# Optimization experiments

Hardware: AMD Instinct MI355X
Metric: run time of the kernel (lower is better)

The kernel has to match this reference:

```python
import jax, jax.numpy as jnp
import numpy as np

T, B, V, D, H = 1024, 128, 50257, 128, 512


def _lstm_cell(x, h, c, w_ih, w_hh, b_ih, b_hh):
    # x: [B, D], h/c: [B, H]; gates: [B, 4H] in PyTorch i,f,g,o order
    gates = x @ w_ih.T + h @ w_hh.T + b_ih + b_hh
    i, f, g, o = jnp.split(gates, 4, axis=-1)
    c_new = jax.nn.sigmoid(f) * c + jax.nn.sigmoid(i) * jnp.tanh(g)
    h_new = jax.nn.sigmoid(o) * jnp.tanh(c_new)
    return h_new, c_new


def setup_inputs() -> dict:
    key = jax.random.key(0)
    ks = jax.random.split(key, 7)
    s = 1.0 / np.sqrt(H)
    return {
        "input_ids": jax.random.randint(ks[0], (T, B), 0, V),
        "seq_len": jnp.sort(jax.random.randint(ks[1], (B,), 0, T)),
        "emb_weight": jax.random.normal(ks[2], (V, D), jnp.float32) * 0.1,
        "w_ih": jax.random.uniform(ks[3], (4 * H, D), jnp.float32, -s, s),
        "w_hh": jax.random.uniform(ks[4], (4 * H, H), jnp.float32, -s, s),
        "b_ih": jax.random.uniform(ks[5], (4 * H,), jnp.float32, -s, s),
        "b_hh": jax.random.uniform(ks[6], (4 * H,), jnp.float32, -s, s),
    }


def reference(input_ids, seq_len, emb_weight, w_ih, w_hh, b_ih, b_hh):
    Tn, Bn = input_ids.shape
    Hn = w_hh.shape[1]
    dt = emb_weight.dtype
    z = jnp.zeros((Bn, Hn), dt)

    def step(carry, inp):
        h, c, last_h, last_c = carry
        t, ids = inp
        x = emb_weight[ids]                       # embedding lookup (dropout=identity, eval)
        h_new, c_new = _lstm_cell(x, h, c, w_ih, w_hh, b_ih, b_hh)
        # hold previously reported features once timestep >= seq_len (skip blend at t==0)
        hold = ((t > 0) & (t >= seq_len)).astype(dt)[:, None]
        blend_c = c_new * (1.0 - hold) + last_c * hold
        blend_h = h_new * (1.0 - hold) + last_h * hold
        # RNN internal state keeps evolving (module is stateful across steps)
        return (h_new, c_new, blend_h, blend_c), None

    (_, _, _, final_c), _ = jax.lax.scan(
        step, (z, z, z, z), (jnp.arange(Tn), input_ids)
    )
    return final_c  # [B, H] mask-blended last cell state
```

## Files before the change

kernel.cpp:

```cpp
#include <hip/hip_runtime.h>

typedef _Float16 half8 __attribute__((ext_vector_type(8)));
typedef float float4v __attribute__((ext_vector_type(4)));
typedef unsigned long long u64;

#define TSEQ  1024
#define BATCH 128
#define HID   512
#define DIN   128

#define HW_STRIDE 264
#define HBUF_WORDS (8 * HW_STRIDE)
#define GOFF (2 * HBUF_WORDS * 4)
#define LDS_BYTES (GOFF + 4 * 8 * 32 * 4)

#define WS_HWORDS_OFF 0
#define WS_BAR_OFF    (2 * BATCH * HID * 4)
#define WS_XALL_OFF   (1u << 20)
#define WS_NEED       ((size_t)WS_XALL_OFF + (size_t)TSEQ * BATCH * DIN * 2)

__device__ inline half8 cvt8(float4v a, float4v b) {
    half8 r;
    r[0] = (_Float16)a[0]; r[1] = (_Float16)a[1];
    r[2] = (_Float16)a[2]; r[3] = (_Float16)a[3];
    r[4] = (_Float16)b[0]; r[5] = (_Float16)b[1];
    r[6] = (_Float16)b[2]; r[7] = (_Float16)b[3];
    return r;
}

__device__ inline float sigm(float x) {
    return __builtin_amdgcn_rcpf(1.0f + __builtin_amdgcn_exp2f(-1.44269504f * x));
}
__device__ inline float tanh_fast(float x) { return 2.0f * sigm(2.0f * x) - 1.0f; }

template <bool XA>
__global__ __launch_bounds__(256, 1)
void lstm_persistent(const int* __restrict__ ids,
                     const int* __restrict__ seq_len,
                     const float* __restrict__ emb,
                     const float* __restrict__ w_ih,
                     const float* __restrict__ w_hh,
                     const float* __restrict__ b_ih,
                     const float* __restrict__ b_hh,
                     float* __restrict__ out,
                     unsigned* __restrict__ h_words,
                     _Float16* __restrict__ x_all,
                     int* __restrict__ bar)
{
    __shared__ __align__(16) char smem[LDS_BYTES];
    unsigned* hsu = (unsigned*)smem;
    _Float16* hsh = (_Float16*)smem;
    float*    gs  = (float*)(smem + GOFF);

    const int tid  = threadIdx.x;
    const int lane = tid & 63;
    const int wv   = tid >> 6;
    const int team = blockIdx.x & 15;
    const int p    = blockIdx.x >> 4;
    const int rowbase   = team * 8;
    const int unit_base = p * 32 + wv * 8;

    const int col  = lane & 15;
    const int kq   = lane >> 4;
    const int arow = lane & 7;
    const int my_row  = lane >> 3;
    const int my_unit = unit_base + (lane & 7);

    if (XA) {
        for (int pair = blockIdx.x * 256 + tid; pair < TSEQ * BATCH;
             pair += 256 * 256) {
            const float* src = emb + (size_t)ids[pair] * DIN;
            _Float16* dst = x_all + (size_t)pair * DIN;
#pragma unroll
            for (int k = 0; k < 16; ++k) {
                float4v a = *(const float4v*)(src + k * 8);
                float4v c = *(const float4v*)(src + k * 8 + 4);
                *(half8*)(dst + k * 8) = cvt8(a, c);
            }
        }
        __threadfence();
        __syncthreads();
        if (tid == 0) {
            __hip_atomic_fetch_add(bar, 1, __ATOMIC_RELEASE,
                                   __HIP_MEMORY_SCOPE_AGENT);
            int g = 0;
            while (__hip_atomic_load(bar, __ATOMIC_ACQUIRE,
                                     __HIP_MEMORY_SCOPE_AGENT) < 256
                   && ++g < (1 << 26)) { }
        }
        __syncthreads();
        __threadfence();
    }

    int tmax = 0, my_tstar = 0;
    for (int r = 0; r < 8; ++r) {
        int s  = seq_len[rowbase + r];
        int ts = (s > 0) ? (s - 1) : 0;
        if (r == my_row) my_tstar = ts;
        tmax = (ts > tmax) ? ts : tmax;
    }

    const int wrow0 = (col & 3) * HID + unit_base + (col >> 2);
    const int wrow1 = (col & 3) * HID + unit_base + 4 + (col >> 2);
    const float bias0 = b_ih[wrow0] + b_hh[wrow0];
    const float bias1 = b_ih[wrow1] + b_hh[wrow1];

    half8 whhf0[16], whhf1[16];
#pragma unroll
    for (int kt = 0; kt < 16; ++kt) {
        const float* s0 = w_hh + (size_t)wrow0 * HID + kt * 32 + kq * 8;
        const float* s1 = w_hh + (size_t)wrow1 * HID + kt * 32 + kq * 8;
        whhf0[kt] = cvt8(*(const float4v*)s0, *(const float4v*)(s0 + 4));
        whhf1[kt] = cvt8(*(const float4v*)s1, *(const float4v*)(s1 + 4));
    }
    half8 wihf0[4], wihf1[4];
#pragma unroll
    for (int kt = 0; kt < 4; ++kt) {
        const float* s0 = w_ih + (size_t)wrow0 * DIN + kt * 32 + kq * 8;
        const float* s1 = w_ih + (size_t)wrow1 * DIN + kt * 32 + kq * 8;
        wihf0[kt] = cvt8(*(const float4v*)s0, *(const float4v*)(s0 + 4));
        wihf1[kt] = cvt8(*(const float4v*)s1, *(const float4v*)(s1 + 4));
    }

    float c_state = 0.0f;
    const int crow = tid >> 5;
    const int coff = tid & 31;

    half8 xf[4], xn[4];
    if (XA) {
        const _Float16* x0 = x_all + ((size_t)0 * BATCH + rowbase + arow) * DIN;
        const int t1 = (tmax > 0) ? 1 : 0;
        const _Float16* x1 = x_all + ((size_t)t1 * BATCH + rowbase + arow) * DIN;
#pragma unroll
        for (int kt = 0; kt < 4; ++kt) {
            xf[kt] = *(const half8*)(x0 + kt * 32 + kq * 8);
            xn[kt] = *(const half8*)(x1 + kt * 32 + kq * 8);
        }
    } else {
        const int id0 = ids[rowbase + arow];
        const float* xrow = emb + (size_t)id0 * DIN;
#pragma unroll
        for (int kt = 0; kt < 4; ++kt) {
            const float* s = xrow + kt * 32 + kq * 8;
            xf[kt] = cvt8(*(const float4v*)s, *(const float4v*)(s + 4));
        }
    }

    const u64 tagmask = 0xFFFF0000FFFF0000ull;

    for (int t = 0; t <= tmax; ++t) {
        int id_next = 0;
        if (!XA) {
            const int tn = (t < tmax) ? (t + 1) : t;
            id_next = ids[tn * BATCH + rowbase + arow];
        }

        float4v acc0a = {bias0, bias0, bias0, bias0};
        float4v acc1a = {bias1, bias1, bias1, bias1};
        float4v acc0b = {0, 0, 0, 0}, acc1b = {0, 0, 0, 0};
#pragma unroll
        for (int kt = 0; kt < 4; ++kt) {
            if (kt & 1) {
                acc0b = __builtin_amdgcn_mfma_f32_16x16x32_f16(xf[kt], wihf0[kt], acc0b, 0, 0, 0);
                acc1b = __builtin_amdgcn_mfma_f32_16x16x32_f16(xf[kt], wihf1[kt], acc1b, 0, 0, 0);
            } else {
                acc0a = __builtin_amdgcn_mfma_f32_16x16x32_f16(xf[kt], wihf0[kt], acc0a, 0, 0, 0);
                acc1a = __builtin_amdgcn_mfma_f32_16x16x32_f16(xf[kt], wihf1[kt], acc1a, 0, 0, 0);
            }
        }

        const int bs = t & 1;
        if (t > 0) {
            const u64* rowp = (const u64*)(h_words
                + (size_t)((t + 1) & 1) * BATCH * HID + (rowbase + crow) * HID);
            const u64 tagpat = ((u64)t << 16) | ((u64)t << 48);
            unsigned* dst = hsu + bs * HBUF_WORDS + crow * HW_STRIDE + coff;
            u64 w[8];
            unsigned pending = 0xFF;
#pragma unroll
            for (int j = 0; j < 8; ++j)
                w[j] = __hip_atomic_load(rowp + coff + 32 * j,
                                         __ATOMIC_RELAXED, __HIP_MEMORY_SCOPE_AGENT);
#pragma unroll
            for (int j = 0; j < 8; ++j) {
                if ((w[j] & tagmask) == tagpat) {
                    dst[32 * j] = (unsigned)(w[j] & 0xFFFFu)
                                | ((unsigned)(w[j] >> 32) << 16);
                    pending &= ~(1u << j);
                }
            }
            int round = 0, guard = 0;
            while (pending) {
#pragma unroll
                for (int j = 0; j < 8; ++j) {
                    if (pending & (1u << j)) {
                        u64 v = __hip_atomic_load(rowp + coff + 32 * j,
                                                  __ATOMIC_RELAXED,
                                                  __HIP_MEMORY_SCOPE_AGENT);
                        if ((v & tagmask) == tagpat) {
                            dst[32 * j] = (unsigned)(v & 0xFFFFu)
                                        | ((unsigned)(v >> 32) << 16);
                            pending &= ~(1u << j);
                        }
                    }
                }
                if (!pending) break;
                if (++round >= 3) __builtin_amdgcn_s_sleep(1);
                if (++guard > (1 << 20)) break;
            }
        }
        __syncthreads();

        float4v xraw[8];
        if (!XA) {
            const float* xrow = emb + (size_t)id_next * DIN;
#pragma unroll
            for (int kt = 0; kt < 4; ++kt) {
                xraw[2 * kt]     = *(const float4v*)(xrow + kt * 32 + kq * 8);
                xraw[2 * kt + 1] = *(const float4v*)(xrow + kt * 32 + kq * 8 + 4);
            }
        }

        if (t > 0) {
            const _Float16* hb = hsh + bs * HBUF_WORDS * 2;
#pragma unroll
            for (int kt = 0; kt < 16; ++kt) {
                half8 af = *(const half8*)(hb + arow * (HW_STRIDE * 2) + kt * 32 + kq * 8);
                if (kt & 1) {
                    acc0b = __builtin_amdgcn_mfma_f32_16x16x32_f16(af, whhf0[kt], acc0b, 0, 0, 0);
                    acc1b = __builtin_amdgcn_mfma_f32_16x16x32_f16(af, whhf1[kt], acc1b, 0, 0, 0);
                } else {
                    acc0a = __builtin_amdgcn_mfma_f32_16x16x32_f16(af, whhf0[kt], acc0a, 0, 0, 0);
                    acc1a = __builtin_amdgcn_mfma_f32_16x16x32_f16(af, whhf1[kt], acc1a, 0, 0, 0);
                }
            }
        }
        const float4v g0 = acc0a + acc0b;
        const float4v g1 = acc1a + acc1b;

        float* gw = gs + wv * 256;
        if (lane < 32) {
            const int grow = (lane >> 4) * 4;
#pragma unroll
            for (int r = 0; r < 4; ++r) {
                gw[(grow + r) * 32 + col]      = g0[r];
                gw[(grow + r) * 32 + 16 + col] = g1[r];
            }
        }
        const float4v g4 = *(const float4v*)(gw + my_row * 32 + (lane & 7) * 4);

        const float i_s = sigm(g4[0]);
        const float f_s = sigm(g4[1]);
        const float g_t = tanh_fast(g4[2]);
        const float o_s = sigm(g4[3]);
        c_state = f_s * c_state + i_s * g_t;
        const float hn = o_s * tanh_fast(c_state);

        if (t == my_tstar)
            out[(rowbase + my_row) * HID + my_unit] = c_state;

        const unsigned short hb16 = __builtin_bit_cast(unsigned short, (_Float16)hn);
        __hip_atomic_store(h_words + (size_t)(t & 1) * BATCH * HID
                                   + (rowbase + my_row) * HID + my_unit,
                           ((unsigned)(t + 1) << 16) | (unsigned)hb16,
                           __ATOMIC_RELAXED, __HIP_MEMORY_SCOPE_AGENT);

        if (XA) {
#pragma unroll
            for (int kt = 0; kt < 4; ++kt) xf[kt] = xn[kt];
            const int t2 = (t + 2 <= tmax) ? (t + 2) : tmax;
            const _Float16* xs2 = x_all + ((size_t)t2 * BATCH + rowbase + arow) * DIN;
#pragma unroll
            for (int kt = 0; kt < 4; ++kt)
                xn[kt] = *(const half8*)(xs2 + kt * 32 + kq * 8);
        } else {
#pragma unroll
            for (int kt = 0; kt < 4; ++kt)
                xf[kt] = cvt8(xraw[2 * kt], xraw[2 * kt + 1]);
        }
    }
}

extern "C" void kernel_launch(void* const* d_in, const int* in_sizes, int n_in,
                              void* d_out, int out_size, void* d_ws, size_t ws_size,
                              hipStream_t stream)
{
    const int*   ids  = (const int*)d_in[0];
    const int*   slen = (const int*)d_in[1];
    const float* emb  = (const float*)d_in[2];
    const float* wih  = (const float*)d_in[3];
    const float* whh  = (const float*)d_in[4];
    const float* bih  = (const float*)d_in[5];
    const float* bhh  = (const float*)d_in[6];
    float* out = (float*)d_out;

    unsigned*  h_words = (unsigned*)((char*)d_ws + WS_HWORDS_OFF);
    int*       bar     = (int*)((char*)d_ws + WS_BAR_OFF);
    _Float16*  x_all   = (_Float16*)((char*)d_ws + WS_XALL_OFF);

    if (ws_size >= WS_NEED) {
        hipMemsetAsync(bar, 0, sizeof(int), stream);
        hipLaunchKernelGGL((lstm_persistent<true>), dim3(256), dim3(256), 0, stream,
                           ids, slen, emb, wih, whh, bih, bhh, out,
                           h_words, x_all, bar);
    } else {
        hipLaunchKernelGGL((lstm_persistent<false>), dim3(256), dim3(256), 0, stream,
                           ids, slen, emb, wih, whh, bih, bhh, out,
                           h_words, x_all, bar);
    }
}
```

Before: 2.081 ms.

## Pack hidden-state exchange into fp16 with phase bit and hoist input MFMAs

Each published hidden value shrinks from a 32-bit word carrying an fp16 value plus a 16-bit step tag to a bare fp16 whose mantissa LSB holds a phase bit that flips every two steps. This halves the cross-block polling traffic and the number of atomic loads, and lets valid data be copied straight into LDS as 64-bit chunks. The input-projection MFMAs for the next step are moved to the end of the loop so they run before the wait for neighbour data, and the recurrent accumulation is split over four accumulator chains. The costs are one lost mantissa bit of h and a weaker staleness check: a single phase bit can accept stale workspace data left over from an earlier launch.

```diff
diff --git a/kernel.cpp b/kernel.cpp
--- a/kernel.cpp
+++ b/kernel.cpp
@@ -14,10 +14,10 @@
 #define GOFF (2 * HBUF_WORDS * 4)
 #define LDS_BYTES (GOFF + 4 * 8 * 32 * 4)
 
-#define WS_HWORDS_OFF 0
-#define WS_BAR_OFF    (2 * BATCH * HID * 4)
-#define WS_XALL_OFF   (1u << 20)
-#define WS_NEED       ((size_t)WS_XALL_OFF + (size_t)TSEQ * BATCH * DIN * 2)
+#define WS_H16_OFF  0
+#define WS_BAR_OFF  (2 * BATCH * HID * 2)
+#define WS_XALL_OFF (1u << 20)
+#define WS_NEED     ((size_t)WS_XALL_OFF + (size_t)TSEQ * BATCH * DIN * 2)
 
 __device__ inline half8 cvt8(float4v a, float4v b) {
     half8 r;
@@ -43,7 +43,7 @@
                      const float* __restrict__ b_ih,
                      const float* __restrict__ b_hh,
                      float* __restrict__ out,
-                     unsigned* __restrict__ h_words,
+                     _Float16* __restrict__ h16,
                      _Float16* __restrict__ x_all,
                      int* __restrict__ bar)
 {
@@ -146,60 +146,55 @@
         }
     }
 
-    const u64 tagmask = 0xFFFF0000FFFF0000ull;
+    float4v a0 = {bias0, bias0, bias0, bias0}, b0 = {0,0,0,0}, c0 = {0,0,0,0}, d0 = {0,0,0,0};
+    float4v a1 = {bias1, bias1, bias1, bias1}, b1 = {0,0,0,0}, c1 = {0,0,0,0}, d1 = {0,0,0,0};
+    a0 = __builtin_amdgcn_mfma_f32_16x16x32_f16(xf[0], wihf0[0], a0, 0, 0, 0);
+    b0 = __builtin_amdgcn_mfma_f32_16x16x32_f16(xf[1], wihf0[1], b0, 0, 0, 0);
+    c0 = __builtin_amdgcn_mfma_f32_16x16x32_f16(xf[2], wihf0[2], c0, 0, 0, 0);
+    d0 = __builtin_amdgcn_mfma_f32_16x16x32_f16(xf[3], wihf0[3], d0, 0, 0, 0);
+    a1 = __builtin_amdgcn_mfma_f32_16x16x32_f16(xf[0], wihf1[0], a1, 0, 0, 0);
+    b1 = __builtin_amdgcn_mfma_f32_16x16x32_f16(xf[1], wihf1[1], b1, 0, 0, 0);
+    c1 = __builtin_amdgcn_mfma_f32_16x16x32_f16(xf[2], wihf1[2], c1, 0, 0, 0);
+    d1 = __builtin_amdgcn_mfma_f32_16x16x32_f16(xf[3], wihf1[3], d1, 0, 0, 0);
+
+    const u64 LSBM = 0x0001000100010001ull;
 
     for (int t = 0; t <= tmax; ++t) {
+        const int bs = t & 1;
         int id_next = 0;
         if (!XA) {
             const int tn = (t < tmax) ? (t + 1) : t;
             id_next = ids[tn * BATCH + rowbase + arow];
         }
 
-        float4v acc0a = {bias0, bias0, bias0, bias0};
-        float4v acc1a = {bias1, bias1, bias1, bias1};
-        float4v acc0b = {0, 0, 0, 0}, acc1b = {0, 0, 0, 0};
-#pragma unroll
-        for (int kt = 0; kt < 4; ++kt) {
-            if (kt & 1) {
-                acc0b = __builtin_amdgcn_mfma_f32_16x16x32_f16(xf[kt], wihf0[kt], acc0b, 0, 0, 0);
-                acc1b = __builtin_amdgcn_mfma_f32_16x16x32_f16(xf[kt], wihf1[kt], acc1b, 0, 0, 0);
-            } else {
-                acc0a = __builtin_amdgcn_mfma_f32_16x16x32_f16(xf[kt], wihf0[kt], acc0a, 0, 0, 0);
-                acc1a = __builtin_amdgcn_mfma_f32_16x16x32_f16(xf[kt], wihf1[kt], acc1a, 0, 0, 0);
-            }
-        }
-
-        const int bs = t & 1;
         if (t > 0) {
-            const u64* rowp = (const u64*)(h_words
+            const u64* rowp = (const u64*)(h16
                 + (size_t)((t + 1) & 1) * BATCH * HID + (rowbase + crow) * HID);
-            const u64 tagpat = ((u64)t << 16) | ((u64)t << 48);
-            unsigned* dst = hsu + bs * HBUF_WORDS + crow * HW_STRIDE + coff;
-            u64 w[8];
-            unsigned pending = 0xFF;
-#pragma unroll
-            for (int j = 0; j < 8; ++j)
-                w[j] = __hip_atomic_load(rowp + coff + 32 * j,
+            const u64 want = ((((t - 1) >> 1) & 1) ^ 1) ? LSBM : 0ull;
+            unsigned* dstw = hsu + bs * HBUF_WORDS + crow * HW_STRIDE + 2 * coff;
+            u64 v[4];
+            unsigned pending = 0xF;
+#pragma unroll
+            for (int j = 0; j < 4; ++j)
+                v[j] = __hip_atomic_load(rowp + coff + 32 * j,
                                          __ATOMIC_RELAXED, __HIP_MEMORY_SCOPE_AGENT);
 #pragma unroll
-            for (int j = 0; j < 8; ++j) {
-                if ((w[j] & tagmask) == tagpat) {
-                    dst[32 * j] = (unsigned)(w[j] & 0xFFFFu)
-                                | ((unsigned)(w[j] >> 32) << 16);
+            for (int j = 0; j < 4; ++j) {
+                if (((v[j] ^ want) & LSBM) == 0) {
+                    *(u64*)(dstw + 64 * j) = v[j];
                     pending &= ~(1u << j);
                 }
             }
             int round = 0, guard = 0;
             while (pending) {
 #pragma unroll
-                for (int j = 0; j < 8; ++j) {
+                for (int j = 0; j < 4; ++j) {
                     if (pending & (1u << j)) {
-                        u64 v = __hip_atomic_load(rowp + coff + 32 * j,
+                        u64 x = __hip_atomic_load(rowp + coff + 32 * j,
                                                   __ATOMIC_RELAXED,
                                                   __HIP_MEMORY_SCOPE_AGENT);
-                        if ((v & tagmask) == tagpat) {
-                            dst[32 * j] = (unsigned)(v & 0xFFFFu)
-                                        | ((unsigned)(v >> 32) << 16);
+                        if (((x ^ want) & LSBM) == 0) {
+                            *(u64*)(dstw + 64 * j) = x;
                             pending &= ~(1u << j);
                         }
                     }
@@ -226,17 +221,27 @@
 #pragma unroll
             for (int kt = 0; kt < 16; ++kt) {
                 half8 af = *(const half8*)(hb + arow * (HW_STRIDE * 2) + kt * 32 + kq * 8);
-                if (kt & 1) {
-                    acc0b = __builtin_amdgcn_mfma_f32_16x16x32_f16(af, whhf0[kt], acc0b, 0, 0, 0);
-                    acc1b = __builtin_amdgcn_mfma_f32_16x16x32_f16(af, whhf1[kt], acc1b, 0, 0, 0);
-                } else {
-                    acc0a = __builtin_amdgcn_mfma_f32_16x16x32_f16(af, whhf0[kt], acc0a, 0, 0, 0);
-                    acc1a = __builtin_amdgcn_mfma_f32_16x16x32_f16(af, whhf1[kt], acc1a, 0, 0, 0);
+                switch (kt & 3) {
+                case 0:
+                    a0 = __builtin_amdgcn_mfma_f32_16x16x32_f16(af, whhf0[kt], a0, 0, 0, 0);
+                    a1 = __builtin_amdgcn_mfma_f32_16x16x32_f16(af, whhf1[kt], a1, 0, 0, 0);
+                    break;
+                case 1:
+                    b0 = __builtin_amdgcn_mfma_f32_16x16x32_f16(af, whhf0[kt], b0, 0, 0, 0);
+                    b1 = __builtin_amdgcn_mfma_f32_16x16x32_f16(af, whhf1[kt], b1, 0, 0, 0);
+                    break;
+                case 2:
+                    c0 = __builtin_amdgcn_mfma_f32_16x16x32_f16(af, whhf0[kt], c0, 0, 0, 0);
+                    c1 = __builtin_amdgcn_mfma_f32_16x16x32_f16(af, whhf1[kt], c1, 0, 0, 0);
+                    break;
+                default:
+                    d0 = __builtin_amdgcn_mfma_f32_16x16x32_f16(af, whhf0[kt], d0, 0, 0, 0);
+                    d1 = __builtin_amdgcn_mfma_f32_16x16x32_f16(af, whhf1[kt], d1, 0, 0, 0);
                 }
             }
         }
-        const float4v g0 = acc0a + acc0b;
-        const float4v g1 = acc1a + acc1b;
+        const float4v g0 = (a0 + b0) + (c0 + d0);
+        const float4v g1 = (a1 + b1) + (c1 + d1);
 
         float* gw = gs + wv * 256;
         if (lane < 32) {
@@ -259,11 +264,15 @@
         if (t == my_tstar)
             out[(rowbase + my_row) * HID + my_unit] = c_state;
 
-        const unsigned short hb16 = __builtin_bit_cast(unsigned short, (_Float16)hn);
-        __hip_atomic_store(h_words + (size_t)(t & 1) * BATCH * HID
+        {
+            const unsigned pub_phase = (((unsigned)t >> 1) & 1u) ^ 1u;
+            unsigned short hb16 = __builtin_bit_cast(unsigned short, (_Float16)hn);
+            hb16 = (unsigned short)((hb16 & 0xFFFEu) | pub_phase);
+            __hip_atomic_store((unsigned short*)h16
+                                   + (size_t)(t & 1) * BATCH * HID
                                    + (rowbase + my_row) * HID + my_unit,
-                           ((unsigned)(t + 1) << 16) | (unsigned)hb16,
-                           __ATOMIC_RELAXED, __HIP_MEMORY_SCOPE_AGENT);
+                               hb16, __ATOMIC_RELAXED, __HIP_MEMORY_SCOPE_AGENT);
+        }
 
         if (XA) {
 #pragma unroll
@@ -278,6 +287,19 @@
             for (int kt = 0; kt < 4; ++kt)
                 xf[kt] = cvt8(xraw[2 * kt], xraw[2 * kt + 1]);
         }
+
+        a0 = (float4v){bias0, bias0, bias0, bias0}; b0 = (float4v){0,0,0,0};
+        c0 = (float4v){0,0,0,0};                    d0 = (float4v){0,0,0,0};
+        a1 = (float4v){bias1, bias1, bias1, bias1}; b1 = (float4v){0,0,0,0};
+        c1 = (float4v){0,0,0,0};                    d1 = (float4v){0,0,0,0};
+        a0 = __builtin_amdgcn_mfma_f32_16x16x32_f16(xf[0], wihf0[0], a0, 0, 0, 0);
+        b0 = __builtin_amdgcn_mfma_f32_16x16x32_f16(xf[1], wihf0[1], b0, 0, 0, 0);
+        c0 = __builtin_amdgcn_mfma_f32_16x16x32_f16(xf[2], wihf0[2], c0, 0, 0, 0);
+        d0 = __builtin_amdgcn_mfma_f32_16x16x32_f16(xf[3], wihf0[3], d0, 0, 0, 0);
+        a1 = __builtin_amdgcn_mfma_f32_16x16x32_f16(xf[0], wihf1[0], a1, 0, 0, 0);
+        b1 = __builtin_amdgcn_mfma_f32_16x16x32_f16(xf[1], wihf1[1], b1, 0, 0, 0);
+        c1 = __builtin_amdgcn_mfma_f32_16x16x32_f16(xf[2], wihf1[2], c1, 0, 0, 0);
+        d1 = __builtin_amdgcn_mfma_f32_16x16x32_f16(xf[3], wihf1[3], d1, 0, 0, 0);
     }
 }
 
@@ -294,18 +316,18 @@
     const float* bhh  = (const float*)d_in[6];
     float* out = (float*)d_out;
 
-    unsigned*  h_words = (unsigned*)((char*)d_ws + WS_HWORDS_OFF);
-    int*       bar     = (int*)((char*)d_ws + WS_BAR_OFF);
-    _Float16*  x_all   = (_Float16*)((char*)d_ws + WS_XALL_OFF);
+    _Float16* h16   = (_Float16*)((char*)d_ws + WS_H16_OFF);
+    int*      bar   = (int*)((char*)d_ws + WS_BAR_OFF);
+    _Float16* x_all = (_Float16*)((char*)d_ws + WS_XALL_OFF);
 
     if (ws_size >= WS_NEED) {
         hipMemsetAsync(bar, 0, sizeof(int), stream);
         hipLaunchKernelGGL((lstm_persistent<true>), dim3(256), dim3(256), 0, stream,
                            ids, slen, emb, wih, whh, bih, bhh, out,
-                           h_words, x_all, bar);
+                           h16, x_all, bar);
     } else {
         hipLaunchKernelGGL((lstm_persistent<false>), dim3(256), dim3(256), 0, stream,
                            ids, slen, emb, wih, whh, bih, bhh, out,
-                           h_words, x_all, bar);
+                           h16, x_all, bar);
     }
 }
```

Result: faster. 1.982 ms (-4.7%).
